# Kernel tuning notes

Hardware: AMD Instinct MI355X
Metric: run time of the kernel (lower is better)

The kernel has to match this reference:

```python
import jax, jax.numpy as jnp
import numpy as np

B, L, H, NH, NB = 8, 200, 128, 4, 2
HD = H // NH
ITEM_NUM, TIME_SPAN = 50000, 256
PAD = -2.0**32 + 1.0


def setup_inputs() -> dict:
    key = jax.random.key(0)
    ks = jax.random.split(key, 32)
    def g(i, shape, s=0.02):
        return jax.random.normal(ks[i], shape, jnp.float32) * s
    item_emb = g(0, (ITEM_NUM + 1, H)).at[0].set(0.0)  # padding_idx=0
    return dict(
        user_ids=jax.random.randint(ks[1], (B,), 0, 1000),
        log_seqs=jax.random.randint(ks[2], (B, L), 0, ITEM_NUM),
        time_matrices=jax.random.randint(ks[3], (B, L, L), 0, TIME_SPAN + 1),
        pos_seqs=jax.random.randint(ks[4], (B, L), 0, ITEM_NUM + 1),
        neg_seqs=jax.random.randint(ks[5], (B, L), 0, ITEM_NUM + 1),
        item_emb=item_emb,
        pos_K_emb=g(6, (L, H)), pos_V_emb=g(7, (L, H)),
        time_K_emb=g(8, (TIME_SPAN + 1, H)), time_V_emb=g(9, (TIME_SPAN + 1, H)),
        attn_ln_g=jnp.ones((NB, H)), attn_ln_b=jnp.zeros((NB, H)),
        Wq=g(10, (NB, H, H)), bq=jnp.zeros((NB, H)),
        Wk=g(11, (NB, H, H)), bk=jnp.zeros((NB, H)),
        Wv=g(12, (NB, H, H)), bv=jnp.zeros((NB, H)),
        fwd_ln_g=jnp.ones((NB, H)), fwd_ln_b=jnp.zeros((NB, H)),
        W1=g(13, (NB, H, H)), b1=jnp.zeros((NB, H)),
        W2=g(14, (NB, H, H)), b2=jnp.zeros((NB, H)),
        last_ln_g=jnp.ones((H,)), last_ln_b=jnp.zeros((H,)),
    )


def _ln(x, g, b, eps=1e-8):
    m = x.mean(-1, keepdims=True)
    v = jnp.var(x, axis=-1, keepdims=True)
    return (x - m) / jnp.sqrt(v + eps) * g + b


def _heads(x):
    # [..., H] -> [NH, ..., HD]; matches torch.cat(torch.split(x, HD, -1), 0)
    y = x.reshape(x.shape[:-1] + (NH, HD))
    return jnp.moveaxis(y, -2, 0)


def reference(user_ids, log_seqs, time_matrices, pos_seqs, neg_seqs, item_emb,
              pos_K_emb, pos_V_emb, time_K_emb, time_V_emb,
              attn_ln_g, attn_ln_b, Wq, bq, Wk, bk, Wv, bv,
              fwd_ln_g, fwd_ln_b, W1, b1, W2, b2, last_ln_g, last_ln_b):
    # user_ids is unused in the original forward as well.
    tmask = log_seqs == 0                                  # [B,L] True = pad
    keep = (~tmask)[..., None].astype(jnp.float32)
    seqs = item_emb[log_seqs] * np.float32(np.sqrt(H))
    seqs = seqs * keep
    pKh = _heads(pos_K_emb)                                # [NH,L,HD]
    pVh = _heads(pos_V_emb)
    tKh = _heads(time_K_emb[time_matrices])                # [NH,B,L,L,HD]
    tVh = _heads(time_V_emb[time_matrices])
    causal = ~jnp.tril(jnp.ones((L, L), bool))             # True above diag -> masked
    bad = tmask[:, :, None] | causal[None]                 # [B,L,L]
    scale = np.float32(np.sqrt(HD))
    for i in range(NB):
        Qin = _ln(seqs, attn_ln_g[i], attn_ln_b[i])
        Qh = _heads(Qin @ Wq[i].T + bq[i])                 # [NH,B,L,HD]
        Kh = _heads(seqs @ Wk[i].T + bk[i])
        Vh = _heads(seqs @ Wv[i].T + bv[i])
        attn = (jnp.einsum('nbqd,nbkd->nbqk', Qh, Kh)
                + jnp.einsum('nbqd,nkd->nbqk', Qh, pKh)
                + jnp.einsum('nbqkd,nbqd->nbqk', tKh, Qh)) / scale
        attn = jnp.where(bad[None], PAD, attn)
        attn = jax.nn.softmax(attn, axis=-1)
        out = (jnp.einsum('nbqk,nbkd->nbqd', attn, Vh)
               + jnp.einsum('nbqk,nkd->nbqd', attn, pVh)
               + jnp.einsum('nbqk,nbqkd->nbqd', attn, tVh))
        out = jnp.moveaxis(out, 0, -2).reshape(seqs.shape)  # merge heads -> [B,L,H]
        seqs = Qin + out                                    # residual uses LN'd Q (as in source)
        seqs = _ln(seqs, fwd_ln_g[i], fwd_ln_b[i])
        ff = jax.nn.relu(seqs @ W1[i].T + b1[i]) @ W2[i].T + b2[i] + seqs
        seqs = ff * keep
    log_feats = _ln(seqs, last_ln_g, last_ln_b)
    pos_logits = (log_feats * item_emb[pos_seqs]).sum(-1)   # [B,L]
    neg_logits = (log_feats * item_emb[neg_seqs]).sum(-1)
    return pos_logits, neg_logits
```

## Files before the change

kernel.cpp:

```cpp
#include <hip/hip_runtime.h>

#define BB 8
#define LL 200
#define HH 128
#define NHEAD 4
#define HDIM 32
#define NBLK 2
#define BL (BB * LL)
#define NT 257
#define QT 8
#define NQT 25
#define SSP 208
#define KTP 66
#define TSP 132

static constexpr float SQRT_H    = 11.313708498984761f;
static constexpr float INV_SCALE = 0.17677669529663687f;
static constexpr float PADV      = -4294967295.0f;

__global__ void k_qkv_gemm(const float* __restrict__ seqs_in,
                           const int* __restrict__ log_seqs,
                           const float* __restrict__ item_emb,
                           const float* __restrict__ g, const float* __restrict__ bia,
                           const float* __restrict__ Wq, const float* __restrict__ bq,
                           const float* __restrict__ Wk, const float* __restrict__ bk,
                           const float* __restrict__ Wv, const float* __restrict__ bv,
                           const float* __restrict__ posK, const float* __restrict__ posV,
                           float* __restrict__ Qin, float* __restrict__ Q,
                           float* __restrict__ K, float* __restrict__ V) {
    int mt = blockIdx.x / 6, ntg = blockIdx.x % 6;
    int nt0 = ntg * 4;
    int matsel = nt0 >> 3;
    int jb0 = (nt0 & 7) * 16;
    int row0 = mt * 32;
    int tid = threadIdx.x;
    __shared__ float As[32 * TSP];
    __shared__ float Bs[2][16 * TSP];

    {
        int r = tid >> 3, seg = tid & 7;
        int row = row0 + r;
        float4 vv[4];
        if (seqs_in) {
            #pragma unroll
            for (int i = 0; i < 4; i++)
                vv[i] = *(const float4*)(seqs_in + (size_t)row * HH + seg * 16 + i * 4);
        } else {
            int idx = log_seqs[row];
            if (idx == 0) {
                #pragma unroll
                for (int i = 0; i < 4; i++) vv[i] = make_float4(0.f, 0.f, 0.f, 0.f);
            } else {
                #pragma unroll
                for (int i = 0; i < 4; i++) {
                    float4 e = *(const float4*)(item_emb + (size_t)idx * HH + seg * 16 + i * 4);
                    vv[i] = make_float4(e.x * SQRT_H, e.y * SQRT_H, e.z * SQRT_H, e.w * SQRT_H);
                }
            }
        }
        if (matsel == 0) {
            float s = 0.f, s2 = 0.f;
            #pragma unroll
            for (int i = 0; i < 4; i++) {
                s  += vv[i].x + vv[i].y + vv[i].z + vv[i].w;
                s2 += vv[i].x * vv[i].x + vv[i].y * vv[i].y + vv[i].z * vv[i].z + vv[i].w * vv[i].w;
            }
            #pragma unroll
            for (int off = 1; off < 8; off <<= 1) {
                s  += __shfl_xor(s, off);
                s2 += __shfl_xor(s2, off);
            }
            float mean = s * (1.f / HH);
            float var  = s2 * (1.f / HH) - mean * mean;
            float inv  = 1.f / sqrtf(var + 1e-8f);
            #pragma unroll
            for (int i = 0; i < 4; i++) {
                int k = seg * 16 + i * 4;
                float4 g4 = *(const float4*)(g + k);
                float4 b4 = *(const float4*)(bia + k);
                float4 y;
                y.x = (vv[i].x - mean) * inv * g4.x + b4.x;
                y.y = (vv[i].y - mean) * inv * g4.y + b4.y;
                y.z = (vv[i].z - mean) * inv * g4.z + b4.z;
                y.w = (vv[i].w - mean) * inv * g4.w + b4.w;
                *(float4*)&As[r * TSP + k] = y;
                if (nt0 == 0) *(float4*)(Qin + (size_t)row * HH + k) = y;
            }
        } else {
            #pragma unroll
            for (int i = 0; i < 4; i++)
                *(float4*)&As[r * TSP + seg * 16 + i * 4] = vv[i];
        }
    }
    const float* W = (matsel == 0) ? Wq : (matsel == 1) ? Wk : Wv;
    int j = tid >> 4, seg16 = tid & 15;
    float4 w0 = *(const float4*)(W + (size_t)(jb0 + j) * HH + seg16 * 8);
    float4 w1 = *(const float4*)(W + (size_t)(jb0 + j) * HH + seg16 * 8 + 4);
    *(float4*)&Bs[0][j * TSP + seg16 * 8]     = w0;
    *(float4*)&Bs[0][j * TSP + seg16 * 8 + 4] = w1;
    __syncthreads();

    int m = tid >> 3, jg = tid & 7;
    const float* ar = &As[m * TSP];
    #pragma unroll
    for (int it = 0; it < 4; it++) {
        int jb = jb0 + it * 16;
        if (it < 3) {
            int jbn = jb0 + (it + 1) * 16;
            w0 = *(const float4*)(W + (size_t)(jbn + j) * HH + seg16 * 8);
            w1 = *(const float4*)(W + (size_t)(jbn + j) * HH + seg16 * 8 + 4);
        }
        float acc0 = 0.f, acc1 = 0.f;
        const float* b0r = &Bs[it & 1][(jg * 2) * TSP];
        const float* b1r = &Bs[it & 1][(jg * 2 + 1) * TSP];
        #pragma unroll 4
        for (int k4 = 0; k4 < 32; k4++) {
            float4 a  = *(const float4*)(ar + k4 * 4);
            float4 b0 = *(const float4*)(b0r + k4 * 4);
            float4 b1 = *(const float4*)(b1r + k4 * 4);
            acc0 += a.x * b0.x + a.y * b0.y + a.z * b0.z + a.w * b0.w;
            acc1 += a.x * b1.x + a.y * b1.y + a.z * b1.z + a.w * b1.w;
        }
        int row = row0 + m;
        int col = jb + jg * 2;
        int l = row % LL;
        if (matsel == 0) {
            float2 bb = *(const float2*)(bq + col);
            *(float2*)(Q + (size_t)row * HH + col) =
                make_float2((acc0 + bb.x) * INV_SCALE, (acc1 + bb.y) * INV_SCALE);
        } else if (matsel == 1) {
            float2 bb = *(const float2*)(bk + col);
            float2 pk = *(const float2*)(posK + (size_t)l * HH + col);
            *(float2*)(K + (size_t)row * HH + col) =
                make_float2(acc0 + bb.x + pk.x, acc1 + bb.y + pk.y);
        } else {
            float2 bb = *(const float2*)(bv + col);
            float2 pv = *(const float2*)(posV + (size_t)l * HH + col);
            *(float2*)(V + (size_t)row * HH + col) =
                make_float2(acc0 + bb.x + pv.x, acc1 + bb.y + pv.y);
        }
        if (it < 3) {
            *(float4*)&Bs[(it + 1) & 1][j * TSP + seg16 * 8]     = w0;
            *(float4*)&Bs[(it + 1) & 1][j * TSP + seg16 * 8 + 4] = w1;
        }
        __syncthreads();
    }
}

__global__ void k_attn(const float* __restrict__ Q, const float* __restrict__ K,
                       const float* __restrict__ V,
                       const float* __restrict__ timeK, const float* __restrict__ timeV,
                       const int* __restrict__ tm,
                       float* __restrict__ att) {
    int bn = blockIdx.x & 31;
    int b = bn >> 2, n = bn & 3;
    int qt = (NQT - 1) - (blockIdx.x >> 5);
    int q0 = qt * QT;
    int kmax = q0 + QT - 1;
    int tid = threadIdx.x;
    int wv = tid >> 6, ln = tid & 63;

    __shared__ float KstT[2][HDIM * KTP];
    __shared__ float DTW[QT * NT];
    __shared__ float Ssc[QT * SSP];
    __shared__ float Ost[QT * HDIM];
    __shared__ int   tmst[QT * LL];

    Ost[tid] = 0.f;
    #pragma unroll
    for (int qi = 0; qi < QT; qi++)
        if (tid < LL)
            tmst[qi * LL + tid] = tm[((size_t)(b * LL + q0 + qi)) * LL + tid];

    int k2 = tid & 31, qi_c = tid >> 5;
    int q = q0 + qi_c;

    float qreg[HDIM];
    {
        const float* qp = Q + ((size_t)(b * LL + q)) * HH + n * HDIM;
        #pragma unroll
        for (int i = 0; i < 8; i++) {
            float4 v = *(const float4*)(qp + i * 4);
            qreg[i * 4 + 0] = v.x; qreg[i * 4 + 1] = v.y;
            qreg[i * 4 + 2] = v.z; qreg[i * 4 + 3] = v.w;
        }
    }

    const int nchS = (kmax >> 6) + 1;
    const int ncht = 5 + nchS;

    int rS = tid >> 3, d4 = tid & 7;

    auto ld_chunk = [&](int c, float4& f0, float4& f1) {
        f0 = make_float4(0.f, 0.f, 0.f, 0.f);
        f1 = make_float4(0.f, 0.f, 0.f, 0.f);
        if (c < 5) {
            int tau = c * 64 + rS;
            if (tau < NT)      f0 = *(const float4*)(timeK + (size_t)tau * HH + n * HDIM + d4 * 4);
            if (tau + 32 < NT) f1 = *(const float4*)(timeK + (size_t)(tau + 32) * HH + n * HDIM + d4 * 4);
        } else {
            int k = (c - 5) * 64 + rS;
            if (k < LL)      f0 = *(const float4*)(K + ((size_t)(b * LL + k)) * HH + n * HDIM + d4 * 4);
            if (k + 32 < LL) f1 = *(const float4*)(K + ((size_t)(b * LL + k + 32)) * HH + n * HDIM + d4 * 4);
        }
    };
    auto wr_chunk = [&](float4 f0, float4 f1, float* buf) {
        buf[(d4 * 4 + 0) * KTP + rS] = f0.x;
        buf[(d4 * 4 + 1) * KTP + rS] = f0.y;
        buf[(d4 * 4 + 2) * KTP + rS] = f0.z;
        buf[(d4 * 4 + 3) * KTP + rS] = f0.w;
        buf[(d4 * 4 + 0) * KTP + rS + 32] = f1.x;
        buf[(d4 * 4 + 1) * KTP + rS + 32] = f1.y;
        buf[(d4 * 4 + 2) * KTP + rS + 32] = f1.z;
        buf[(d4 * 4 + 3) * KTP + rS + 32] = f1.w;
    };

    {
        float4 c0, c1;
        ld_chunk(0, c0, c1);
        wr_chunk(c0, c1, KstT[0]);
    }
    __syncthreads();
    for (int c = 0; c < ncht; c++) {
        float4 n0, n1;
        bool more = (c + 1 < ncht);
        if (more) ld_chunk(c + 1, n0, n1);
        const float* buf = KstT[c & 1];
        float a0 = 0.f, a1 = 0.f;
        #pragma unroll 4
        for (int d = 0; d < HDIM; d++) {
            float qv = qreg[d];
            float2 kv = *(const float2*)&buf[d * KTP + k2 * 2];
            a0 += qv * kv.x; a1 += qv * kv.y;
        }
        if (c < 5) {
            int tau0 = c * 64 + k2 * 2;
            if (tau0 < NT)     DTW[qi_c * NT + tau0]     = a0;
            if (tau0 + 1 < NT) DTW[qi_c * NT + tau0 + 1] = a1;
        } else {
            int k0 = (c - 5) * 64 + k2 * 2;
            if (k0 <= kmax)     Ssc[qi_c * SSP + k0]     = a0;
            if (k0 + 1 <= kmax) Ssc[qi_c * SSP + k0 + 1] = a1;
        }
        if (more) wr_chunk(n0, n1, KstT[(c + 1) & 1]);
        __syncthreads();
    }

    for (int rr = 0; rr < 2; rr++) {
        int qi = wv + rr * 4;
        int qq = q0 + qi;
        float sv[4];
        float m = PADV;
        #pragma unroll
        for (int jj = 0; jj < 4; jj++) {
            int k = ln + 64 * jj;
            sv[jj] = (k <= qq) ? (Ssc[qi * SSP + k] + DTW[qi * NT + tmst[qi * LL + k]]) : PADV;
            m = fmaxf(m, sv[jj]);
        }
        for (int off = 32; off; off >>= 1) m = fmaxf(m, __shfl_xor(m, off));
        float sum = 0.f;
        #pragma unroll
        for (int jj = 0; jj < 4; jj++) {
            int k = ln + 64 * jj;
            sv[jj] = (k <= qq) ? __expf(sv[jj] - m) : 0.f;
            sum += sv[jj];
        }
        for (int off = 32; off; off >>= 1) sum += __shfl_xor(sum, off);
        float inv = 1.f / sum;
        #pragma unroll
        for (int jj = 0; jj < 4; jj++) {
            int k = ln + 64 * jj;
            if (k < SSP) Ssc[qi * SSP + k] = (k <= qq) ? sv[jj] * inv : 0.f;
        }
    }
    __syncthreads();

    int d = tid & 31, kg = tid >> 5;
    float acc[QT] = {0,0,0,0,0,0,0,0};
    const float* vb  = V + ((size_t)(b * LL)) * HH + n * HDIM + d;
    const float* tvb = timeV + n * HDIM + d;
    for (int k = kg; k <= kmax; k += 8) {
        float v = vb[(size_t)k * HH];
        #pragma unroll
        for (int qi = 0; qi < QT; qi++) {
            float p  = Ssc[qi * SSP + k];
            float tv = tvb[(size_t)tmst[qi * LL + k] * HH];
            acc[qi] += p * (v + tv);
        }
    }
    #pragma unroll
    for (int qi = 0; qi < QT; qi++) atomicAdd(&Ost[qi * HDIM + d], acc[qi]);
    __syncthreads();
    {
        int qi = tid >> 5;
        att[((size_t)(b * LL + q0 + qi)) * HH + n * HDIM + (tid & 31)] = Ost[tid];
    }
}

__global__ void k_ff1(const float* __restrict__ Qin, const float* __restrict__ att,
                      const float* __restrict__ g, const float* __restrict__ bia,
                      const float* __restrict__ W1, const float* __restrict__ b1,
                      float* __restrict__ h1) {
    int mt = blockIdx.x >> 1, jb0 = (blockIdx.x & 1) * 64;
    int row0 = mt * 16;
    int tid = threadIdx.x;
    __shared__ float As[16 * TSP];
    __shared__ float Bs[2][16 * TSP];

    {
        int r = tid >> 4, seg = tid & 15;
        int row = row0 + r;
        float4 vv[2];
        #pragma unroll
        for (int i = 0; i < 2; i++) {
            int k = seg * 8 + i * 4;
            float4 q4 = *(const float4*)(Qin + (size_t)row * HH + k);
            float4 a4 = *(const float4*)(att + (size_t)row * HH + k);
            vv[i] = make_float4(q4.x + a4.x, q4.y + a4.y, q4.z + a4.z, q4.w + a4.w);
        }
        float s = 0.f, s2 = 0.f;
        #pragma unroll
        for (int i = 0; i < 2; i++) {
            s  += vv[i].x + vv[i].y + vv[i].z + vv[i].w;
            s2 += vv[i].x * vv[i].x + vv[i].y * vv[i].y + vv[i].z * vv[i].z + vv[i].w * vv[i].w;
        }
        #pragma unroll
        for (int off = 1; off < 16; off <<= 1) {
            s  += __shfl_xor(s, off);
            s2 += __shfl_xor(s2, off);
        }
        float mean = s * (1.f / HH);
        float var  = s2 * (1.f / HH) - mean * mean;
        float inv  = 1.f / sqrtf(var + 1e-8f);
        #pragma unroll
        for (int i = 0; i < 2; i++) {
            int k = seg * 8 + i * 4;
            float4 g4 = *(const float4*)(g + k);
            float4 b4 = *(const float4*)(bia + k);
            float4 y;
            y.x = (vv[i].x - mean) * inv * g4.x + b4.x;
            y.y = (vv[i].y - mean) * inv * g4.y + b4.y;
            y.z = (vv[i].z - mean) * inv * g4.z + b4.z;
            y.w = (vv[i].w - mean) * inv * g4.w + b4.w;
            *(float4*)&As[r * TSP + k] = y;
        }
    }
    int j = tid >> 4, seg16 = tid & 15;
    float4 w0 = *(const float4*)(W1 + (size_t)(jb0 + j) * HH + seg16 * 8);
    float4 w1 = *(const float4*)(W1 + (size_t)(jb0 + j) * HH + seg16 * 8 + 4);
    *(float4*)&Bs[0][j * TSP + seg16 * 8]     = w0;
    *(float4*)&Bs[0][j * TSP + seg16 * 8 + 4] = w1;
    __syncthreads();

    int m = tid >> 4, jj = tid & 15;
    const float* ar = &As[m * TSP];
    #pragma unroll
    for (int it = 0; it < 4; it++) {
        int jb = jb0 + it * 16;
        if (it < 3) {
            int jbn = jb0 + (it + 1) * 16;
            w0 = *(const float4*)(W1 + (size_t)(jbn + j) * HH + seg16 * 8);
            w1 = *(const float4*)(W1 + (size_t)(jbn + j) * HH + seg16 * 8 + 4);
        }
        float acc = 0.f;
        const float* br = &Bs[it & 1][jj * TSP];
        #pragma unroll 4
        for (int k4 = 0; k4 < 32; k4++) {
            float4 a = *(const float4*)(ar + k4 * 4);
            float4 b = *(const float4*)(br + k4 * 4);
            acc += a.x * b.x + a.y * b.y + a.z * b.z + a.w * b.w;
        }
        int col = jb + jj;
        float t = acc + b1[col];
        h1[(size_t)(row0 + m) * HH + col] = t > 0.f ? t : 0.f;
        if (it < 3) {
            *(float4*)&Bs[(it + 1) & 1][j * TSP + seg16 * 8]     = w0;
            *(float4*)&Bs[(it + 1) & 1][j * TSP + seg16 * 8 + 4] = w1;
        }
        __syncthreads();
    }
}

__global__ void k_ff2(const float* __restrict__ h1,
                      const float* __restrict__ Qin, const float* __restrict__ att,
                      const float* __restrict__ g, const float* __restrict__ bia,
                      const float* __restrict__ W2, const float* __restrict__ b2,
                      const int* __restrict__ log_seqs,
                      float* __restrict__ out) {
    int mt = blockIdx.x >> 1, jb0 = (blockIdx.x & 1) * 64;
    int row0 = mt * 16;
    int tid = threadIdx.x;
    __shared__ float As[16 * TSP];
    __shared__ float Bs[2][16 * TSP];
    __shared__ float mu[16], rstd[16];

    {
        int r = tid >> 4, seg = tid & 15;
        int row = row0 + r;
        #pragma unroll
        for (int i = 0; i < 2; i++) {
            int k = seg * 8 + i * 4;
            *(float4*)&As[r * TSP + k] = *(const float4*)(h1 + (size_t)row * HH + k);
        }
        float s = 0.f, s2 = 0.f;
        #pragma unroll
        for (int i = 0; i < 2; i++) {
            int k = seg * 8 + i * 4;
            float4 q4 = *(const float4*)(Qin + (size_t)row * HH + k);
            float4 a4 = *(const float4*)(att + (size_t)row * HH + k);
            float4 v = make_float4(q4.x + a4.x, q4.y + a4.y, q4.z + a4.z, q4.w + a4.w);
            s  += v.x + v.y + v.z + v.w;
            s2 += v.x * v.x + v.y * v.y + v.z * v.z + v.w * v.w;
        }
        #pragma unroll
        for (int off = 1; off < 16; off <<= 1) {
            s  += __shfl_xor(s, off);
            s2 += __shfl_xor(s2, off);
        }
        float mean = s * (1.f / HH);
        float var  = s2 * (1.f / HH) - mean * mean;
        if (seg == 0) { mu[r] = mean; rstd[r] = 1.f / sqrtf(var + 1e-8f); }
    }
    int j = tid >> 4, seg16 = tid & 15;
    float4 w0 = *(const float4*)(W2 + (size_t)(jb0 + j) * HH + seg16 * 8);
    float4 w1 = *(const float4*)(W2 + (size_t)(jb0 + j) * HH + seg16 * 8 + 4);
    *(float4*)&Bs[0][j * TSP + seg16 * 8]     = w0;
    *(float4*)&Bs[0][j * TSP + seg16 * 8 + 4] = w1;
    __syncthreads();

    int m = tid >> 4, jj = tid & 15;
    const float* ar = &As[m * TSP];
    #pragma unroll
    for (int it = 0; it < 4; it++) {
        int jb = jb0 + it * 16;
        if (it < 3) {
            int jbn = jb0 + (it + 1) * 16;
            w0 = *(const float4*)(W2 + (size_t)(jbn + j) * HH + seg16 * 8);
            w1 = *(const float4*)(W2 + (size_t)(jbn + j) * HH + seg16 * 8 + 4);
        }
        float acc = 0.f;
        const float* br = &Bs[it & 1][jj * TSP];
        #pragma unroll 4
        for (int k4 = 0; k4 < 32; k4++) {
            float4 a = *(const float4*)(ar + k4 * 4);
            float4 b = *(const float4*)(br + k4 * 4);
            acc += a.x * b.x + a.y * b.y + a.z * b.z + a.w * b.w;
        }
        int row = row0 + m;
        int col = jb + jj;
        float resid = Qin[(size_t)row * HH + col] + att[(size_t)row * HH + col];
        float y = (resid - mu[m]) * rstd[m] * g[col] + bia[col];
        float o = acc + b2[col] + y;
        if (log_seqs[row] == 0) o = 0.f;
        out[(size_t)row * HH + col] = o;
        if (it < 3) {
            *(float4*)&Bs[(it + 1) & 1][j * TSP + seg16 * 8]     = w0;
            *(float4*)&Bs[(it + 1) & 1][j * TSP + seg16 * 8 + 4] = w1;
        }
        __syncthreads();
    }
}

__global__ void k_lnlogits(const float* __restrict__ seqs,
                           const float* __restrict__ g, const float* __restrict__ bia,
                           const float* __restrict__ item_emb,
                           const int* __restrict__ pos, const int* __restrict__ neg,
                           float* __restrict__ out) {
    int row = blockIdx.x;
    int h = threadIdx.x;
    float v = seqs[(size_t)row * HH + h];
    float s = v, s2 = v * v;
    for (int off = 32; off; off >>= 1) {
        s  += __shfl_xor(s, off);
        s2 += __shfl_xor(s2, off);
    }
    __shared__ float r1[2], r2[2];
    if ((h & 63) == 0) { r1[h >> 6] = s; r2[h >> 6] = s2; }
    __syncthreads();
    float mean = (r1[0] + r1[1]) * (1.f / HH);
    float var  = (r2[0] + r2[1]) * (1.f / HH) - mean * mean;
    float inv = 1.f / sqrtf(var + 1e-8f);
    float f = (v - mean) * inv * g[h] + bia[h];

    int ip = pos[row], in_ = neg[row];
    float vp = f * item_emb[(size_t)ip * HH + h];
    float vn = f * item_emb[(size_t)in_ * HH + h];
    for (int off = 32; off; off >>= 1) {
        vp += __shfl_xor(vp, off);
        vn += __shfl_xor(vn, off);
    }
    __shared__ float rp[2], rn[2];
    if ((h & 63) == 0) { rp[h >> 6] = vp; rn[h >> 6] = vn; }
    __syncthreads();
    if (h == 0) {
        out[row]      = rp[0] + rp[1];
        out[BL + row] = rn[0] + rn[1];
    }
}

extern "C" void kernel_launch(void* const* d_in, const int* in_sizes, int n_in,
                              void* d_out, int out_size, void* d_ws, size_t ws_size,
                              hipStream_t stream) {
    const int* log_seqs   = (const int*)d_in[1];
    const int* tm         = (const int*)d_in[2];
    const int* pos_seqs   = (const int*)d_in[3];
    const int* neg_seqs   = (const int*)d_in[4];
    const float* item_emb = (const float*)d_in[5];
    const float* posK     = (const float*)d_in[6];
    const float* posV     = (const float*)d_in[7];
    const float* timeK    = (const float*)d_in[8];
    const float* timeV    = (const float*)d_in[9];
    const float* attn_g   = (const float*)d_in[10];
    const float* attn_b   = (const float*)d_in[11];
    const float* Wq       = (const float*)d_in[12];
    const float* bq       = (const float*)d_in[13];
    const float* Wk       = (const float*)d_in[14];
    const float* bk       = (const float*)d_in[15];
    const float* Wv       = (const float*)d_in[16];
    const float* bv       = (const float*)d_in[17];
    const float* fwd_g    = (const float*)d_in[18];
    const float* fwd_b    = (const float*)d_in[19];
    const float* W1       = (const float*)d_in[20];
    const float* b1       = (const float*)d_in[21];
    const float* W2       = (const float*)d_in[22];
    const float* b2       = (const float*)d_in[23];
    const float* last_g   = (const float*)d_in[24];
    const float* last_b   = (const float*)d_in[25];

    float* seqs = (float*)d_ws;
    float* Qin  = seqs + (size_t)BL * HH;
    float* Qb   = Qin  + (size_t)BL * HH;
    float* Kb   = Qb   + (size_t)BL * HH;
    float* Vb   = Kb   + (size_t)BL * HH;
    float* att  = Vb   + (size_t)BL * HH;
    float* h1   = att  + (size_t)BL * HH;

    for (int i = 0; i < NBLK; i++) {
        k_qkv_gemm<<<300, 256, 0, stream>>>(i == 0 ? nullptr : seqs, log_seqs, item_emb,
                                            attn_g + i * HH, attn_b + i * HH,
                                            Wq + (size_t)i * HH * HH, bq + i * HH,
                                            Wk + (size_t)i * HH * HH, bk + i * HH,
                                            Wv + (size_t)i * HH * HH, bv + i * HH,
                                            posK, posV, Qin, Qb, Kb, Vb);
        k_attn<<<NQT * 32, 256, 0, stream>>>(Qb, Kb, Vb, timeK, timeV, tm, att);
        k_ff1<<<200, 256, 0, stream>>>(Qin, att, fwd_g + i * HH, fwd_b + i * HH,
                                       W1 + (size_t)i * HH * HH, b1 + i * HH, h1);
        k_ff2<<<200, 256, 0, stream>>>(h1, Qin, att, fwd_g + i * HH, fwd_b + i * HH,
                                       W2 + (size_t)i * HH * HH, b2 + i * HH,
                                       log_seqs, seqs);
    }
    k_lnlogits<<<BL, HH, 0, stream>>>(seqs, last_g, last_b, item_emb,
                                      pos_seqs, neg_seqs, (float*)d_out);
}
```

Baseline: 235.1 us.

## Fuse FF1 and FF2 into one kernel and fold final LayerNorm logits

Merges the two feed-forward GEMM kernels into one kernel per block. The hidden activation stays in shared memory instead of going through a global h1 buffer, and the layer-normed residual is reused from shared memory. For the last block, the final LayerNorm and the pos/neg logit dot products are fused into the same kernel, which removes the separate logits launch. The grid halves from 200 to 100 workgroups, each computing all 128 output columns, so parallelism drops on a GPU with many CUs in exchange for fewer launches and less global traffic.

```diff
diff --git a/kernel.cpp b/kernel.cpp
--- a/kernel.cpp
+++ b/kernel.cpp
@@ -297,14 +297,21 @@
     }
 }
 
-__global__ void k_ff1(const float* __restrict__ Qin, const float* __restrict__ att,
-                      const float* __restrict__ g, const float* __restrict__ bia,
-                      const float* __restrict__ W1, const float* __restrict__ b1,
-                      float* __restrict__ h1) {
-    int mt = blockIdx.x >> 1, jb0 = (blockIdx.x & 1) * 64;
-    int row0 = mt * 16;
+template <int LAST>
+__device__ __forceinline__ void ff_body(
+        const float* __restrict__ Qin, const float* __restrict__ att,
+        const float* __restrict__ g, const float* __restrict__ bia,
+        const float* __restrict__ W1, const float* __restrict__ b1,
+        const float* __restrict__ W2, const float* __restrict__ b2,
+        const int* __restrict__ log_seqs, float* __restrict__ out,
+        const float* __restrict__ last_g, const float* __restrict__ last_b,
+        const float* __restrict__ item_emb,
+        const int* __restrict__ pos, const int* __restrict__ neg,
+        float* __restrict__ logits) {
+    int row0 = blockIdx.x * 16;
     int tid = threadIdx.x;
     __shared__ float As[16 * TSP];
+    __shared__ float Hs[16 * TSP];
     __shared__ float Bs[2][16 * TSP];
 
     {
@@ -346,8 +353,8 @@
         }
     }
     int j = tid >> 4, seg16 = tid & 15;
-    float4 w0 = *(const float4*)(W1 + (size_t)(jb0 + j) * HH + seg16 * 8);
-    float4 w1 = *(const float4*)(W1 + (size_t)(jb0 + j) * HH + seg16 * 8 + 4);
+    float4 w0 = *(const float4*)(W1 + (size_t)j * HH + seg16 * 8);
+    float4 w1 = *(const float4*)(W1 + (size_t)j * HH + seg16 * 8 + 4);
     *(float4*)&Bs[0][j * TSP + seg16 * 8]     = w0;
     *(float4*)&Bs[0][j * TSP + seg16 * 8 + 4] = w1;
     __syncthreads();
@@ -355,12 +362,12 @@
     int m = tid >> 4, jj = tid & 15;
     const float* ar = &As[m * TSP];
     #pragma unroll
-    for (int it = 0; it < 4; it++) {
-        int jb = jb0 + it * 16;
-        if (it < 3) {
-            int jbn = jb0 + (it + 1) * 16;
-            w0 = *(const float4*)(W1 + (size_t)(jbn + j) * HH + seg16 * 8);
-            w1 = *(const float4*)(W1 + (size_t)(jbn + j) * HH + seg16 * 8 + 4);
+    for (int it = 0; it < 8; it++) {
+        {
+            const float* Wn = (it < 7) ? W1 : W2;
+            int jbn = (it < 7) ? (it + 1) * 16 : 0;
+            w0 = *(const float4*)(Wn + (size_t)(jbn + j) * HH + seg16 * 8);
+            w1 = *(const float4*)(Wn + (size_t)(jbn + j) * HH + seg16 * 8 + 4);
         }
         float acc = 0.f;
         const float* br = &Bs[it & 1][jj * TSP];
@@ -370,71 +377,20 @@
             float4 b = *(const float4*)(br + k4 * 4);
             acc += a.x * b.x + a.y * b.y + a.z * b.z + a.w * b.w;
         }
-        int col = jb + jj;
+        int col = it * 16 + jj;
         float t = acc + b1[col];
-        h1[(size_t)(row0 + m) * HH + col] = t > 0.f ? t : 0.f;
-        if (it < 3) {
-            *(float4*)&Bs[(it + 1) & 1][j * TSP + seg16 * 8]     = w0;
-            *(float4*)&Bs[(it + 1) & 1][j * TSP + seg16 * 8 + 4] = w1;
-        }
+        Hs[m * TSP + col] = t > 0.f ? t : 0.f;
+        *(float4*)&Bs[(it + 1) & 1][j * TSP + seg16 * 8]     = w0;
+        *(float4*)&Bs[(it + 1) & 1][j * TSP + seg16 * 8 + 4] = w1;
         __syncthreads();
     }
-}
-
-__global__ void k_ff2(const float* __restrict__ h1,
-                      const float* __restrict__ Qin, const float* __restrict__ att,
-                      const float* __restrict__ g, const float* __restrict__ bia,
-                      const float* __restrict__ W2, const float* __restrict__ b2,
-                      const int* __restrict__ log_seqs,
-                      float* __restrict__ out) {
-    int mt = blockIdx.x >> 1, jb0 = (blockIdx.x & 1) * 64;
-    int row0 = mt * 16;
-    int tid = threadIdx.x;
-    __shared__ float As[16 * TSP];
-    __shared__ float Bs[2][16 * TSP];
-    __shared__ float mu[16], rstd[16];
-
-    {
-        int r = tid >> 4, seg = tid & 15;
-        int row = row0 + r;
-        #pragma unroll
-        for (int i = 0; i < 2; i++) {
-            int k = seg * 8 + i * 4;
-            *(float4*)&As[r * TSP + k] = *(const float4*)(h1 + (size_t)row * HH + k);
-        }
-        float s = 0.f, s2 = 0.f;
-        #pragma unroll
-        for (int i = 0; i < 2; i++) {
-            int k = seg * 8 + i * 4;
-            float4 q4 = *(const float4*)(Qin + (size_t)row * HH + k);
-            float4 a4 = *(const float4*)(att + (size_t)row * HH + k);
-            float4 v = make_float4(q4.x + a4.x, q4.y + a4.y, q4.z + a4.z, q4.w + a4.w);
-            s  += v.x + v.y + v.z + v.w;
-            s2 += v.x * v.x + v.y * v.y + v.z * v.z + v.w * v.w;
-        }
-        #pragma unroll
-        for (int off = 1; off < 16; off <<= 1) {
-            s  += __shfl_xor(s, off);
-            s2 += __shfl_xor(s2, off);
-        }
-        float mean = s * (1.f / HH);
-        float var  = s2 * (1.f / HH) - mean * mean;
-        if (seg == 0) { mu[r] = mean; rstd[r] = 1.f / sqrtf(var + 1e-8f); }
-    }
-    int j = tid >> 4, seg16 = tid & 15;
-    float4 w0 = *(const float4*)(W2 + (size_t)(jb0 + j) * HH + seg16 * 8);
-    float4 w1 = *(const float4*)(W2 + (size_t)(jb0 + j) * HH + seg16 * 8 + 4);
-    *(float4*)&Bs[0][j * TSP + seg16 * 8]     = w0;
-    *(float4*)&Bs[0][j * TSP + seg16 * 8 + 4] = w1;
-    __syncthreads();
-
-    int m = tid >> 4, jj = tid & 15;
-    const float* ar = &As[m * TSP];
+    const float* hr = &Hs[m * TSP];
+    int row = row0 + m;
+    int dead = (log_seqs[row] == 0);
     #pragma unroll
-    for (int it = 0; it < 4; it++) {
-        int jb = jb0 + it * 16;
-        if (it < 3) {
-            int jbn = jb0 + (it + 1) * 16;
+    for (int it = 0; it < 8; it++) {
+        if (it < 7) {
+            int jbn = (it + 1) * 16;
             w0 = *(const float4*)(W2 + (size_t)(jbn + j) * HH + seg16 * 8);
             w1 = *(const float4*)(W2 + (size_t)(jbn + j) * HH + seg16 * 8 + 4);
         }
@@ -442,60 +398,93 @@
         const float* br = &Bs[it & 1][jj * TSP];
         #pragma unroll 4
         for (int k4 = 0; k4 < 32; k4++) {
-            float4 a = *(const float4*)(ar + k4 * 4);
+            float4 a = *(const float4*)(hr + k4 * 4);
             float4 b = *(const float4*)(br + k4 * 4);
             acc += a.x * b.x + a.y * b.y + a.z * b.z + a.w * b.w;
         }
-        int row = row0 + m;
-        int col = jb + jj;
-        float resid = Qin[(size_t)row * HH + col] + att[(size_t)row * HH + col];
-        float y = (resid - mu[m]) * rstd[m] * g[col] + bia[col];
-        float o = acc + b2[col] + y;
-        if (log_seqs[row] == 0) o = 0.f;
-        out[(size_t)row * HH + col] = o;
-        if (it < 3) {
+        int col = it * 16 + jj;
+        float o = acc + b2[col] + As[m * TSP + col];
+        if (dead) o = 0.f;
+        if (LAST) {
+            As[m * TSP + col] = o;
+        } else {
+            out[(size_t)row * HH + col] = o;
+        }
+        if (it < 7) {
             *(float4*)&Bs[(it + 1) & 1][j * TSP + seg16 * 8]     = w0;
             *(float4*)&Bs[(it + 1) & 1][j * TSP + seg16 * 8 + 4] = w1;
         }
         __syncthreads();
     }
+    if (LAST) {
+        int r = tid >> 4, seg = tid & 15;
+        int lrow = row0 + r;
+        float4 v0 = *(float4*)&As[r * TSP + seg * 8];
+        float4 v1 = *(float4*)&As[r * TSP + seg * 8 + 4];
+        float s  = v0.x + v0.y + v0.z + v0.w + v1.x + v1.y + v1.z + v1.w;
+        float s2 = v0.x * v0.x + v0.y * v0.y + v0.z * v0.z + v0.w * v0.w
+                 + v1.x * v1.x + v1.y * v1.y + v1.z * v1.z + v1.w * v1.w;
+        #pragma unroll
+        for (int off = 1; off < 16; off <<= 1) {
+            s  += __shfl_xor(s, off);
+            s2 += __shfl_xor(s2, off);
+        }
+        float mean = s * (1.f / HH);
+        float var  = s2 * (1.f / HH) - mean * mean;
+        float inv  = 1.f / sqrtf(var + 1e-8f);
+        int ip = pos[lrow], in_ = neg[lrow];
+        const float* pe = item_emb + (size_t)ip * HH + seg * 8;
+        const float* ne = item_emb + (size_t)in_ * HH + seg * 8;
+        float4 lg0 = *(const float4*)(last_g + seg * 8);
+        float4 lg1 = *(const float4*)(last_g + seg * 8 + 4);
+        float4 lb0 = *(const float4*)(last_b + seg * 8);
+        float4 lb1 = *(const float4*)(last_b + seg * 8 + 4);
+        float4 p0 = *(const float4*)(pe),  p1 = *(const float4*)(pe + 4);
+        float4 n0 = *(const float4*)(ne),  n1 = *(const float4*)(ne + 4);
+        float f0 = (v0.x - mean) * inv * lg0.x + lb0.x;
+        float f1 = (v0.y - mean) * inv * lg0.y + lb0.y;
+        float f2 = (v0.z - mean) * inv * lg0.z + lb0.z;
+        float f3 = (v0.w - mean) * inv * lg0.w + lb0.w;
+        float f4 = (v1.x - mean) * inv * lg1.x + lb1.x;
+        float f5 = (v1.y - mean) * inv * lg1.y + lb1.y;
+        float f6 = (v1.z - mean) * inv * lg1.z + lb1.z;
+        float f7 = (v1.w - mean) * inv * lg1.w + lb1.w;
+        float vp = f0 * p0.x + f1 * p0.y + f2 * p0.z + f3 * p0.w
+                 + f4 * p1.x + f5 * p1.y + f6 * p1.z + f7 * p1.w;
+        float vn = f0 * n0.x + f1 * n0.y + f2 * n0.z + f3 * n0.w
+                 + f4 * n1.x + f5 * n1.y + f6 * n1.z + f7 * n1.w;
+        #pragma unroll
+        for (int off = 1; off < 16; off <<= 1) {
+            vp += __shfl_xor(vp, off);
+            vn += __shfl_xor(vn, off);
+        }
+        if (seg == 0) {
+            logits[lrow]      = vp;
+            logits[BL + lrow] = vn;
+        }
+    }
 }
 
-__global__ void k_lnlogits(const float* __restrict__ seqs,
-                           const float* __restrict__ g, const float* __restrict__ bia,
-                           const float* __restrict__ item_emb,
-                           const int* __restrict__ pos, const int* __restrict__ neg,
-                           float* __restrict__ out) {
-    int row = blockIdx.x;
-    int h = threadIdx.x;
-    float v = seqs[(size_t)row * HH + h];
-    float s = v, s2 = v * v;
-    for (int off = 32; off; off >>= 1) {
-        s  += __shfl_xor(s, off);
-        s2 += __shfl_xor(s2, off);
-    }
-    __shared__ float r1[2], r2[2];
-    if ((h & 63) == 0) { r1[h >> 6] = s; r2[h >> 6] = s2; }
-    __syncthreads();
-    float mean = (r1[0] + r1[1]) * (1.f / HH);
-    float var  = (r2[0] + r2[1]) * (1.f / HH) - mean * mean;
-    float inv = 1.f / sqrtf(var + 1e-8f);
-    float f = (v - mean) * inv * g[h] + bia[h];
-
-    int ip = pos[row], in_ = neg[row];
-    float vp = f * item_emb[(size_t)ip * HH + h];
-    float vn = f * item_emb[(size_t)in_ * HH + h];
-    for (int off = 32; off; off >>= 1) {
-        vp += __shfl_xor(vp, off);
-        vn += __shfl_xor(vn, off);
-    }
-    __shared__ float rp[2], rn[2];
-    if ((h & 63) == 0) { rp[h >> 6] = vp; rn[h >> 6] = vn; }
-    __syncthreads();
-    if (h == 0) {
-        out[row]      = rp[0] + rp[1];
-        out[BL + row] = rn[0] + rn[1];
-    }
+__global__ void k_ff(const float* __restrict__ Qin, const float* __restrict__ att,
+                     const float* __restrict__ g, const float* __restrict__ bia,
+                     const float* __restrict__ W1, const float* __restrict__ b1,
+                     const float* __restrict__ W2, const float* __restrict__ b2,
+                     const int* __restrict__ log_seqs, float* __restrict__ out) {
+    ff_body<0>(Qin, att, g, bia, W1, b1, W2, b2, log_seqs, out,
+               nullptr, nullptr, nullptr, nullptr, nullptr, nullptr);
+}
+
+__global__ void k_fflast(const float* __restrict__ Qin, const float* __restrict__ att,
+                         const float* __restrict__ g, const float* __restrict__ bia,
+                         const float* __restrict__ W1, const float* __restrict__ b1,
+                         const float* __restrict__ W2, const float* __restrict__ b2,
+                         const int* __restrict__ log_seqs,
+                         const float* __restrict__ last_g, const float* __restrict__ last_b,
+                         const float* __restrict__ item_emb,
+                         const int* __restrict__ pos, const int* __restrict__ neg,
+                         float* __restrict__ logits) {
+    ff_body<1>(Qin, att, g, bia, W1, b1, W2, b2, log_seqs, nullptr,
+               last_g, last_b, item_emb, pos, neg, logits);
 }
 
 extern "C" void kernel_launch(void* const* d_in, const int* in_sizes, int n_in,
@@ -533,7 +522,6 @@
     float* Kb   = Qb   + (size_t)BL * HH;
     float* Vb   = Kb   + (size_t)BL * HH;
     float* att  = Vb   + (size_t)BL * HH;
-    float* h1   = att  + (size_t)BL * HH;
 
     for (int i = 0; i < NBLK; i++) {
         k_qkv_gemm<<<300, 256, 0, stream>>>(i == 0 ? nullptr : seqs, log_seqs, item_emb,
@@ -543,12 +531,17 @@
                                             Wv + (size_t)i * HH * HH, bv + i * HH,
                                             posK, posV, Qin, Qb, Kb, Vb);
         k_attn<<<NQT * 32, 256, 0, stream>>>(Qb, Kb, Vb, timeK, timeV, tm, att);
-        k_ff1<<<200, 256, 0, stream>>>(Qin, att, fwd_g + i * HH, fwd_b + i * HH,
-                                       W1 + (size_t)i * HH * HH, b1 + i * HH, h1);
-        k_ff2<<<200, 256, 0, stream>>>(h1, Qin, att, fwd_g + i * HH, fwd_b + i * HH,
-                                       W2 + (size_t)i * HH * HH, b2 + i * HH,
-                                       log_seqs, seqs);
-    }
-    k_lnlogits<<<BL, HH, 0, stream>>>(seqs, last_g, last_b, item_emb,
-                                      pos_seqs, neg_seqs, (float*)d_out);
+        if (i < NBLK - 1) {
+            k_ff<<<100, 256, 0, stream>>>(Qin, att, fwd_g + i * HH, fwd_b + i * HH,
+                                          W1 + (size_t)i * HH * HH, b1 + i * HH,
+                                          W2 + (size_t)i * HH * HH, b2 + i * HH,
+                                          log_seqs, seqs);
+        } else {
+            k_fflast<<<100, 256, 0, stream>>>(Qin, att, fwd_g + i * HH, fwd_b + i * HH,
+                                              W1 + (size_t)i * HH * HH, b1 + i * HH,
+                                              W2 + (size_t)i * HH * HH, b2 + i * HH,
+                                              log_seqs, last_g, last_b, item_emb,
+                                              pos_seqs, neg_seqs, (float*)d_out);
+        }
+    }
 }
```

After: 244.6 us. 4.0% more time.

## Rewrite attention score and PV phases with shuffle-reduced dots and per-query accumulation

Applied to the files above, without the earlier changes.

The score phase no longer stages transposed K/timeK chunks in double-buffered shared memory. Each group of 8 lanes now loads one K or timeK row directly, dots it against all 8 queries held in registers, and reduces with warp shuffles. The PV phase gives each query its own wave slice with 4 independent accumulators, which removes the shared-memory atomicAdd reduction and the extra barrier. Block ordering changes from heaviest-first to natural order, and the DTW row stride is padded. The trade-off is more shuffle instructions and possible load imbalance between causal query rows.

```diff
diff --git a/kernel.cpp b/kernel.cpp
--- a/kernel.cpp
+++ b/kernel.cpp
@@ -8,10 +8,10 @@
 #define NBLK 2
 #define BL (BB * LL)
 #define NT 257
+#define NTP 264
 #define QT 8
 #define NQT 25
 #define SSP 208
-#define KTP 66
 #define TSP 132
 
 static constexpr float SQRT_H    = 11.313708498984761f;
@@ -154,98 +154,51 @@
                        float* __restrict__ att) {
     int bn = blockIdx.x & 31;
     int b = bn >> 2, n = bn & 3;
-    int qt = (NQT - 1) - (blockIdx.x >> 5);
+    int qt = blockIdx.x >> 5;
     int q0 = qt * QT;
     int kmax = q0 + QT - 1;
     int tid = threadIdx.x;
-    int wv = tid >> 6, ln = tid & 63;
-
-    __shared__ float KstT[2][HDIM * KTP];
-    __shared__ float DTW[QT * NT];
+
+    __shared__ float DTW[QT * NTP];
     __shared__ float Ssc[QT * SSP];
-    __shared__ float Ost[QT * HDIM];
     __shared__ int   tmst[QT * LL];
 
-    Ost[tid] = 0.f;
     #pragma unroll
     for (int qi = 0; qi < QT; qi++)
         if (tid < LL)
             tmst[qi * LL + tid] = tm[((size_t)(b * LL + q0 + qi)) * LL + tid];
 
-    int k2 = tid & 31, qi_c = tid >> 5;
-    int q = q0 + qi_c;
-
-    float qreg[HDIM];
-    {
-        const float* qp = Q + ((size_t)(b * LL + q)) * HH + n * HDIM;
-        #pragma unroll
-        for (int i = 0; i < 8; i++) {
-            float4 v = *(const float4*)(qp + i * 4);
-            qreg[i * 4 + 0] = v.x; qreg[i * 4 + 1] = v.y;
-            qreg[i * 4 + 2] = v.z; qreg[i * 4 + 3] = v.w;
-        }
-    }
-
-    const int nchS = (kmax >> 6) + 1;
-    const int ncht = 5 + nchS;
-
-    int rS = tid >> 3, d4 = tid & 7;
-
-    auto ld_chunk = [&](int c, float4& f0, float4& f1) {
-        f0 = make_float4(0.f, 0.f, 0.f, 0.f);
-        f1 = make_float4(0.f, 0.f, 0.f, 0.f);
-        if (c < 5) {
-            int tau = c * 64 + rS;
-            if (tau < NT)      f0 = *(const float4*)(timeK + (size_t)tau * HH + n * HDIM + d4 * 4);
-            if (tau + 32 < NT) f1 = *(const float4*)(timeK + (size_t)(tau + 32) * HH + n * HDIM + d4 * 4);
-        } else {
-            int k = (c - 5) * 64 + rS;
-            if (k < LL)      f0 = *(const float4*)(K + ((size_t)(b * LL + k)) * HH + n * HDIM + d4 * 4);
-            if (k + 32 < LL) f1 = *(const float4*)(K + ((size_t)(b * LL + k + 32)) * HH + n * HDIM + d4 * 4);
-        }
-    };
-    auto wr_chunk = [&](float4 f0, float4 f1, float* buf) {
-        buf[(d4 * 4 + 0) * KTP + rS] = f0.x;
-        buf[(d4 * 4 + 1) * KTP + rS] = f0.y;
-        buf[(d4 * 4 + 2) * KTP + rS] = f0.z;
-        buf[(d4 * 4 + 3) * KTP + rS] = f0.w;
-        buf[(d4 * 4 + 0) * KTP + rS + 32] = f1.x;
-        buf[(d4 * 4 + 1) * KTP + rS + 32] = f1.y;
-        buf[(d4 * 4 + 2) * KTP + rS + 32] = f1.z;
-        buf[(d4 * 4 + 3) * KTP + rS + 32] = f1.w;
-    };
-
-    {
-        float4 c0, c1;
-        ld_chunk(0, c0, c1);
-        wr_chunk(c0, c1, KstT[0]);
-    }
-    __syncthreads();
-    for (int c = 0; c < ncht; c++) {
-        float4 n0, n1;
-        bool more = (c + 1 < ncht);
-        if (more) ld_chunk(c + 1, n0, n1);
-        const float* buf = KstT[c & 1];
-        float a0 = 0.f, a1 = 0.f;
-        #pragma unroll 4
-        for (int d = 0; d < HDIM; d++) {
-            float qv = qreg[d];
-            float2 kv = *(const float2*)&buf[d * KTP + k2 * 2];
-            a0 += qv * kv.x; a1 += qv * kv.y;
-        }
-        if (c < 5) {
-            int tau0 = c * 64 + k2 * 2;
-            if (tau0 < NT)     DTW[qi_c * NT + tau0]     = a0;
-            if (tau0 + 1 < NT) DTW[qi_c * NT + tau0 + 1] = a1;
-        } else {
-            int k0 = (c - 5) * 64 + k2 * 2;
-            if (k0 <= kmax)     Ssc[qi_c * SSP + k0]     = a0;
-            if (k0 + 1 <= kmax) Ssc[qi_c * SSP + k0 + 1] = a1;
-        }
-        if (more) wr_chunk(n0, n1, KstT[(c + 1) & 1]);
-        __syncthreads();
-    }
-
+    int g8 = tid >> 3, seg = tid & 7;
+    float4 qf[QT];
+    #pragma unroll
+    for (int qi = 0; qi < QT; qi++)
+        qf[qi] = *(const float4*)(Q + ((size_t)(b * LL + q0 + qi)) * HH + n * HDIM + seg * 4);
+
+    const int R = NT + kmax + 1;
+    for (int row = g8; row < R; row += 32) {
+        const float* src = (row < NT)
+            ? timeK + (size_t)row * HH + n * HDIM + seg * 4
+            : K + ((size_t)(b * LL + (row - NT))) * HH + n * HDIM + seg * 4;
+        float4 v = *(const float4*)src;
+        float p[QT];
+        #pragma unroll
+        for (int qi = 0; qi < QT; qi++)
+            p[qi] = v.x * qf[qi].x + v.y * qf[qi].y + v.z * qf[qi].z + v.w * qf[qi].w;
+        #pragma unroll
+        for (int qi = 0; qi < QT; qi++) {
+            p[qi] += __shfl_xor(p[qi], 1);
+            p[qi] += __shfl_xor(p[qi], 2);
+            p[qi] += __shfl_xor(p[qi], 4);
+        }
+        float out = p[0];
+        #pragma unroll
+        for (int qi = 1; qi < QT; qi++) out = (seg == qi) ? p[qi] : out;
+        if (row < NT) DTW[seg * NTP + row] = out;
+        else          Ssc[seg * SSP + (row - NT)] = out;
+    }
+    __syncthreads();
+
+    int wv = tid >> 6, ln = tid & 63;
     for (int rr = 0; rr < 2; rr++) {
         int qi = wv + rr * 4;
         int qq = q0 + qi;
@@ -254,7 +207,7 @@
         #pragma unroll
         for (int jj = 0; jj < 4; jj++) {
             int k = ln + 64 * jj;
-            sv[jj] = (k <= qq) ? (Ssc[qi * SSP + k] + DTW[qi * NT + tmst[qi * LL + k]]) : PADV;
+            sv[jj] = (k <= qq) ? (Ssc[qi * SSP + k] + DTW[qi * NTP + tmst[qi * LL + k]]) : PADV;
             m = fmaxf(m, sv[jj]);
         }
         for (int off = 32; off; off >>= 1) m = fmaxf(m, __shfl_xor(m, off));
@@ -275,26 +228,23 @@
     }
     __syncthreads();
 
-    int d = tid & 31, kg = tid >> 5;
-    float acc[QT] = {0,0,0,0,0,0,0,0};
+    int d = tid & 31, qi = tid >> 5;
+    int qq = q0 + qi;
     const float* vb  = V + ((size_t)(b * LL)) * HH + n * HDIM + d;
     const float* tvb = timeV + n * HDIM + d;
-    for (int k = kg; k <= kmax; k += 8) {
-        float v = vb[(size_t)k * HH];
-        #pragma unroll
-        for (int qi = 0; qi < QT; qi++) {
-            float p  = Ssc[qi * SSP + k];
-            float tv = tvb[(size_t)tmst[qi * LL + k] * HH];
-            acc[qi] += p * (v + tv);
-        }
-    }
-    #pragma unroll
-    for (int qi = 0; qi < QT; qi++) atomicAdd(&Ost[qi * HDIM + d], acc[qi]);
-    __syncthreads();
-    {
-        int qi = tid >> 5;
-        att[((size_t)(b * LL + q0 + qi)) * HH + n * HDIM + (tid & 31)] = Ost[tid];
-    }
+    const float* pr  = &Ssc[qi * SSP];
+    const int*   tr  = &tmst[qi * LL];
+    float a0 = 0.f, a1 = 0.f, a2 = 0.f, a3 = 0.f;
+    int k = 0;
+    for (; k + 3 <= qq; k += 4) {
+        a0 += pr[k]     * (vb[(size_t)(k)     * HH] + tvb[(size_t)tr[k]     * HH]);
+        a1 += pr[k + 1] * (vb[(size_t)(k + 1) * HH] + tvb[(size_t)tr[k + 1] * HH]);
+        a2 += pr[k + 2] * (vb[(size_t)(k + 2) * HH] + tvb[(size_t)tr[k + 2] * HH]);
+        a3 += pr[k + 3] * (vb[(size_t)(k + 3) * HH] + tvb[(size_t)tr[k + 3] * HH]);
+    }
+    for (; k <= qq; k++)
+        a0 += pr[k] * (vb[(size_t)k * HH] + tvb[(size_t)tr[k] * HH]);
+    att[((size_t)(b * LL + q0 + qi)) * HH + n * HDIM + d] = (a0 + a1) + (a2 + a3);
 }
 
 __global__ void k_ff1(const float* __restrict__ Qin, const float* __restrict__ att,
```

Measured after the change: 238.4 us. About the same (+1.4%).
